# Kernel optimization log

Measured on AMD Instinct MI355X. Metric: run time of the kernel, lower is better.

Reference implementation:

```python
import jax, jax.numpy as jnp
import numpy as np

B, N, FDIM, REL, H = 4, 256, 256, 16, 8
D = FDIM // H


def setup_inputs() -> dict:
    key = jax.random.key(0)
    ks = jax.random.split(key, 10)
    s_f = 1.0 / np.sqrt(FDIM)
    s_kv = 1.0 / np.sqrt(FDIM + REL)
    return {
        "node_features": jax.random.normal(ks[0], (B, N, FDIM), jnp.float32),
        "relative_positions": jax.random.normal(ks[1], (B, N, N, REL), jnp.float32),
        # torch Linear weights stored transposed -> here [in, out]
        "Wq": jax.random.uniform(ks[2], (FDIM, FDIM), jnp.float32, -s_f, s_f),
        "bq": jax.random.uniform(ks[3], (FDIM,), jnp.float32, -s_f, s_f),
        "Wk": jax.random.uniform(ks[4], (FDIM + REL, FDIM), jnp.float32, -s_kv, s_kv),
        "bk": jax.random.uniform(ks[5], (FDIM,), jnp.float32, -s_kv, s_kv),
        "Wv": jax.random.uniform(ks[6], (FDIM + REL, FDIM), jnp.float32, -s_kv, s_kv),
        "bv": jax.random.uniform(ks[7], (FDIM,), jnp.float32, -s_kv, s_kv),
        "Wo": jax.random.uniform(ks[8], (FDIM, FDIM), jnp.float32, -s_f, s_f),
        "bo": jax.random.uniform(ks[9], (FDIM,), jnp.float32, -s_f, s_f),
    }


def reference(node_features, relative_positions, Wq, bq, Wk, bk, Wv, bv, Wo, bo):
    b, n, f = node_features.shape
    # Q: [b, n_i, H, D]
    Q = (node_features @ Wq + bq).reshape(b, n, H, D)
    # per-edge K/V input: [b, i, j, f+rel] where feature part is node j's features
    nf_j = jnp.broadcast_to(node_features[:, None, :, :], (b, n, n, f))
    kv_in = jnp.concatenate([nf_j, relative_positions], axis=-1)
    K = (kv_in @ Wk + bk).reshape(b, n, n, H, D)  # [b, i, j, h, d]
    V = (kv_in @ Wv + bv).reshape(b, n, n, H, D)
    scale = 1.0 / jnp.sqrt(jnp.asarray(D, node_features.dtype))
    scores = jnp.einsum('bihd,bijhd->bhij', Q, K) * scale
    attn = jax.nn.softmax(scores, axis=-1)
    wv = jnp.einsum('bhij,bijhd->bihd', attn, V).reshape(b, n, f)
    return node_features + (wv @ Wo + bo)
```

## Files before the change

### kernel.cpp

```cpp
#include <hip/hip_runtime.h>


#define BB 4
#define NN 256
#define FD 256
#define RL 16
#define NH 8
#define HD 32
#define QI 4

typedef __attribute__((ext_vector_type(8))) short bf16x8;
typedef __attribute__((ext_vector_type(4))) float f32x4;

#define OFF_QB   0
#define OFF_KNA  131072
#define OFF_VNT  262144
#define OFF_NFB  393216
#define OFF_WT   524288

static __device__ __forceinline__ unsigned short f2bf(float x) {
  unsigned int u = __float_as_uint(x);
  unsigned int r = (u + 0x7fffu + ((u >> 16) & 1u)) >> 16;
  return (unsigned short)r;
}
static __device__ __forceinline__ float bf2f(unsigned short h) {
  return __uint_as_float(((unsigned int)h) << 16);
}

__global__ __launch_bounds__(256) void k_prep(
    const float* __restrict__ nf,
    const float* __restrict__ Wq, const float* __restrict__ Wk,
    const float* __restrict__ Wv, const float* __restrict__ Wo,
    float* __restrict__ ws) {
  const int tid = threadIdx.x;
  const int sel = blockIdx.y;
  if (sel == 4) {
    unsigned short* nfB = (unsigned short*)(ws + OFF_NFB);
    const int base = blockIdx.x * 16384;
    #pragma unroll 8
    for (int k = 0; k < 64; ++k) {
      const int idx = base + k * 256 + tid;
      nfB[idx] = f2bf(nf[idx]);
    }
    return;
  }
  const float* W = (sel == 0) ? Wq : (sel == 1) ? Wk : (sel == 2) ? Wv : Wo;
  unsigned short* WT = (unsigned short*)(ws + OFF_WT) + sel * FD * FD;
  __shared__ unsigned short t[64][72];
  const int tx = blockIdx.x & 3, ty = blockIdx.x >> 2;
  const int cx = tid & 63, r0 = tid >> 6;
  #pragma unroll
  for (int rr = r0; rr < 64; rr += 4)
    t[rr][cx] = f2bf(W[(ty * 64 + rr) * FD + tx * 64 + cx]);
  __syncthreads();
  #pragma unroll
  for (int rr = r0; rr < 64; rr += 4)
    WT[(tx * 64 + rr) * FD + ty * 64 + cx] = t[cx][rr];
}

__global__ __launch_bounds__(256) void k_proj(
    const float* __restrict__ bq, const float* __restrict__ bk,
    const float* __restrict__ bv, float* __restrict__ ws) {
  const unsigned short* nfB = (const unsigned short*)(ws + OFF_NFB);
  const int mat = blockIdx.y >> 2;
  const int c0 = (blockIdx.y & 3) * 64;
  const int m0 = blockIdx.x * 64 + (threadIdx.x >> 6) * 16;
  const int l = threadIdx.x & 63;
  const unsigned short* WT = (const unsigned short*)(ws + OFF_WT) + mat * FD * FD;
  const int ar = l & 15, kg = l >> 4;
  f32x4 acc[4];
  #pragma unroll
  for (int nt = 0; nt < 4; ++nt) acc[nt] = (f32x4){0.f, 0.f, 0.f, 0.f};
  #pragma unroll
  for (int ks = 0; ks < 8; ++ks) {
    bf16x8 a = *(const bf16x8*)(nfB + (m0 + ar) * FD + ks * 32 + kg * 8);
    #pragma unroll
    for (int nt = 0; nt < 4; ++nt) {
      bf16x8 b = *(const bf16x8*)(WT + (c0 + nt * 16 + ar) * FD + ks * 32 + kg * 8);
      acc[nt] = __builtin_amdgcn_mfma_f32_16x16x32_bf16(a, b, acc[nt], 0, 0, 0);
    }
  }
  if (mat == 0) {
    const float scale = 0.17677669529663687f;
    unsigned short* Qb = (unsigned short*)(ws + OFF_QB);
    #pragma unroll
    for (int nt = 0; nt < 4; ++nt) {
      const int cc = c0 + nt * 16 + ar;
      const float bb = bq[cc];
      #pragma unroll
      for (int i = 0; i < 4; ++i)
        Qb[(m0 + kg * 4 + i) * FD + cc] = f2bf((acc[nt][i] + bb) * scale);
    }
  } else if (mat == 1) {
    unsigned short* Kn = (unsigned short*)(ws + OFF_KNA);
    #pragma unroll
    for (int nt = 0; nt < 4; ++nt) {
      const int cc = c0 + nt * 16 + ar;
      const float bb = bk[cc];
      #pragma unroll
      for (int i = 0; i < 4; ++i)
        Kn[(m0 + kg * 4 + i) * FD + cc] = f2bf(acc[nt][i] + bb);
    }
  } else {
    unsigned short* VnT = (unsigned short*)(ws + OFF_VNT);
    const int b2 = m0 >> 8, j0 = (m0 & 255) + kg * 4;
    #pragma unroll
    for (int nt = 0; nt < 4; ++nt) {
      const int cc = c0 + nt * 16 + ar;
      const float bb = bv[cc];
      ushort4 v;
      v.x = f2bf(acc[nt][0] + bb); v.y = f2bf(acc[nt][1] + bb);
      v.z = f2bf(acc[nt][2] + bb); v.w = f2bf(acc[nt][3] + bb);
      *(ushort4*)&VnT[((size_t)b2 * FD + cc) * NN + j0] = v;
    }
  }
}

__global__ __launch_bounds__(512, 2) void k_attn11(
    const float* __restrict__ rel,
    const float* __restrict__ Wk,
    const float* __restrict__ Wv,
    const float* __restrict__ nf,
    const float* __restrict__ bo,
    float* __restrict__ out,
    float* __restrict__ ws) {
  const unsigned short* QbG = (const unsigned short*)(ws + OFF_QB);
  const unsigned short* KnG = (const unsigned short*)(ws + OFF_KNA);
  const unsigned short* VTG = (const unsigned short*)(ws + OFF_VNT);
  const unsigned short* WoT = (const unsigned short*)(ws + OFF_WT) + 3 * FD * FD;

  const int bid = (blockIdx.x & 7) * 32 + (blockIdx.x >> 3);
  const int b  = bid >> 6;
  const int i0 = (bid & 63) * QI;
  const int tid = threadIdx.x;
  const int l = tid & 63, w = tid >> 6;
  const int l15 = l & 15, kg = l >> 4;

  __shared__ unsigned short Qb_l[QI * 264];
  __shared__ unsigned short relT[QI * 16 * 264];
  __shared__ unsigned short srelP2[8 * 1064];
  __shared__ float qr_l[QI * 8 * 16];
  __shared__ float ar_l[QI * 8 * 16];
  __shared__ unsigned short wv_l[QI * 264];

  {
    const int t2 = tid * 2, row = t2 >> 8, col = t2 & 255;
    *(unsigned int*)&Qb_l[row * 264 + col] =
        *(const unsigned int*)(QbG + ((size_t)(b * NN + i0 + row)) * FD + col);
  }
  #pragma unroll
  for (int m = 0; m < 2; ++m) {
    const int p = tid + 512 * m, i = p >> 8, j = p & 255;
    const float4* rp = (const float4*)(rel + (((size_t)(b * NN + i0 + i)) * NN + j) * RL);
    #pragma unroll
    for (int q4 = 0; q4 < 4; ++q4) {
      float4 v = rp[q4];
      relT[(i * 16 + q4 * 4 + 0) * 264 + j] = f2bf(v.x);
      relT[(i * 16 + q4 * 4 + 1) * 264 + j] = f2bf(v.y);
      relT[(i * 16 + q4 * 4 + 2) * 264 + j] = f2bf(v.z);
      relT[(i * 16 + q4 * 4 + 3) * 264 + j] = f2bf(v.w);
    }
  }
  __syncthreads();

  {
    const int i = tid >> 7, h = (tid >> 4) & 7, r = tid & 15;
    const unsigned int* qp = (const unsigned int*)&Qb_l[i * 264 + h * 32];
    const float* wrow = Wk + (FD + r) * FD + h * HD;
    float s = 0.f;
    #pragma unroll
    for (int d2 = 0; d2 < 16; ++d2) {
      unsigned int u = qp[d2];
      s += bf2f((unsigned short)(u & 0xffffu)) * wrow[2 * d2];
      s += bf2f((unsigned short)(u >> 16)) * wrow[2 * d2 + 1];
    }
    qr_l[(i * 8 + h) * 16 + r] = s;
  }
  __syncthreads();

  {
    const int i = w & 3, jh = w >> 2;
    const int j0 = jh * 128 + l;
    float rv0[16], rv1[16];
    #pragma unroll
    for (int r = 0; r < 16; ++r) {
      rv0[r] = bf2f(relT[(i * 16 + r) * 264 + j0]);
      rv1[r] = bf2f(relT[(i * 16 + r) * 264 + j0 + 64]);
    }
    #pragma unroll
    for (int h = 0; h < 8; ++h) {
      const float* qv = &qr_l[(i * 8 + h) * 16];
      float s0 = 0.f, s1 = 0.f;
      #pragma unroll
      for (int r = 0; r < 16; ++r) { s0 += qv[r] * rv0[r]; s1 += qv[r] * rv1[r]; }
      srelP2[(i * 8 + h) * 264 + j0]      = f2bf(s0);
      srelP2[(i * 8 + h) * 264 + j0 + 64] = f2bf(s1);
    }
  }
  __syncthreads();

  const int h = w;
  f32x4 acc[16];
  {
    bf16x8 afrag = *(const bf16x8*)&Qb_l[(l15 & 3) * 264 + h * 32 + kg * 8];
    #pragma unroll
    for (int nt = 0; nt < 16; ++nt) {
      bf16x8 bfrag = *(const bf16x8*)(KnG + ((size_t)(b * NN + nt * 16 + l15)) * FD
                                      + h * 32 + kg * 8);
      acc[nt] = __builtin_amdgcn_mfma_f32_16x16x32_bf16(
          afrag, bfrag, (f32x4){0.f, 0.f, 0.f, 0.f}, 0, 0, 0);
    }
    #pragma unroll
    for (int nt = 0; nt < 16; ++nt) {
      #pragma unroll
      for (int ireg = 0; ireg < 4; ++ireg) {
        const int iC = (kg * 4 + ireg) & 3;
        acc[nt][ireg] += bf2f(srelP2[(iC * 8 + h) * 264 + nt * 16 + l15]);
      }
    }
  }
  #pragma unroll
  for (int ireg = 0; ireg < 4; ++ireg) {
    float mx = acc[0][ireg];
    #pragma unroll
    for (int nt = 1; nt < 16; ++nt) mx = fmaxf(mx, acc[nt][ireg]);
    mx = fmaxf(mx, __shfl_xor(mx, 1)); mx = fmaxf(mx, __shfl_xor(mx, 2));
    mx = fmaxf(mx, __shfl_xor(mx, 4)); mx = fmaxf(mx, __shfl_xor(mx, 8));
    float sum = 0.f;
    #pragma unroll
    for (int nt = 0; nt < 16; ++nt) {
      float e = __expf(acc[nt][ireg] - mx);
      acc[nt][ireg] = e; sum += e;
    }
    sum += __shfl_xor(sum, 1); sum += __shfl_xor(sum, 2);
    sum += __shfl_xor(sum, 4); sum += __shfl_xor(sum, 8);
    const float rec = 1.f / sum;
    #pragma unroll
    for (int nt = 0; nt < 16; ++nt) acc[nt][ireg] *= rec;
  }
  __syncthreads();

  if (l < 16) {
    #pragma unroll
    for (int nt = 0; nt < 16; ++nt)
      #pragma unroll
      for (int ireg = 0; ireg < 4; ++ireg)
        srelP2[h * 1064 + ireg * 264 + nt * 16 + l] = f2bf(acc[nt][ireg]);
  }
  __syncthreads();

  if (w < 4) {
    const int i = w;
    const int colh = l15 & 7;
    f32x4 aa = (f32x4){0.f, 0.f, 0.f, 0.f};
    #pragma unroll
    for (int ks = 0; ks < 8; ++ks) {
      bf16x8 a = *(const bf16x8*)&relT[(i * 16 + l15) * 264 + ks * 32 + kg * 8];
      bf16x8 bb = *(const bf16x8*)&srelP2[colh * 1064 + i * 264 + ks * 32 + kg * 8];
      aa = __builtin_amdgcn_mfma_f32_16x16x32_bf16(a, bb, aa, 0, 0, 0);
    }
    if (l15 < 8) {
      #pragma unroll
      for (int ireg = 0; ireg < 4; ++ireg)
        ar_l[(i * 8 + l15) * 16 + kg * 4 + ireg] = aa[ireg];
    }
  }
  __syncthreads();

  {
    const int c = tid & 255, ii0 = tid >> 8, hc = c >> 5;
    float wvv[16];
    #pragma unroll
    for (int r = 0; r < 16; ++r) wvv[r] = Wv[(FD + r) * FD + c];
    #pragma unroll
    for (int k2 = 0; k2 < 2; ++k2) {
      const int i = ii0 + 2 * k2;
      const float* ap = &ar_l[(i * 8 + hc) * 16];
      float s = 0.f;
      #pragma unroll
      for (int r = 0; r < 16; ++r) s += ap[r] * wvv[r];
      wv_l[i * 264 + c] = f2bf(s);
    }
  }
  __syncthreads();

  {
    const int coli = l15 & 3;
    f32x4 o0 = (f32x4){0.f, 0.f, 0.f, 0.f};
    f32x4 o1 = (f32x4){0.f, 0.f, 0.f, 0.f};
    #pragma unroll
    for (int ks = 0; ks < 8; ++ks) {
      bf16x8 bb = *(const bf16x8*)&srelP2[h * 1064 + coli * 264 + ks * 32 + kg * 8];
      bf16x8 a0 = *(const bf16x8*)(VTG + ((size_t)(b * FD + h * 32 + l15)) * NN
                                   + ks * 32 + kg * 8);
      bf16x8 a1 = *(const bf16x8*)(VTG + ((size_t)(b * FD + h * 32 + 16 + l15)) * NN
                                   + ks * 32 + kg * 8);
      o0 = __builtin_amdgcn_mfma_f32_16x16x32_bf16(a0, bb, o0, 0, 0, 0);
      o1 = __builtin_amdgcn_mfma_f32_16x16x32_bf16(a1, bb, o1, 0, 0, 0);
    }
    if (l15 < 4) {
      #pragma unroll
      for (int ireg = 0; ireg < 4; ++ireg) {
        const int c0_ = h * 32 + kg * 4 + ireg;
        const int c1_ = c0_ + 16;
        const int idx0 = l15 * 264 + c0_;
        const int idx1 = l15 * 264 + c1_;
        wv_l[idx0] = f2bf(bf2f(wv_l[idx0]) + o0[ireg]);
        wv_l[idx1] = f2bf(bf2f(wv_l[idx1]) + o1[ireg]);
      }
    }
  }
  __syncthreads();

  {
    const int c0_ = w * 32;
    f32x4 oa0 = (f32x4){0.f, 0.f, 0.f, 0.f};
    f32x4 oa1 = (f32x4){0.f, 0.f, 0.f, 0.f};
    #pragma unroll
    for (int ks = 0; ks < 8; ++ks) {
      bf16x8 a = *(const bf16x8*)&wv_l[(l15 & 3) * 264 + ks * 32 + kg * 8];
      bf16x8 b0 = *(const bf16x8*)(WoT + (c0_ + l15) * FD + ks * 32 + kg * 8);
      bf16x8 b1 = *(const bf16x8*)(WoT + (c0_ + 16 + l15) * FD + ks * 32 + kg * 8);
      oa0 = __builtin_amdgcn_mfma_f32_16x16x32_bf16(a, b0, oa0, 0, 0, 0);
      oa1 = __builtin_amdgcn_mfma_f32_16x16x32_bf16(a, b1, oa1, 0, 0, 0);
    }
    if (l < 16) {
      #pragma unroll
      for (int ireg = 0; ireg < 4; ++ireg) {
        const int row = (b * NN + i0 + ireg) * FD;
        const int cc0 = c0_ + l, cc1 = c0_ + 16 + l;
        out[row + cc0] = nf[row + cc0] + oa0[ireg] + bo[cc0];
        out[row + cc1] = nf[row + cc1] + oa1[ireg] + bo[cc1];
      }
    }
  }
}

extern "C" void kernel_launch(void* const* d_in, const int* in_sizes, int n_in,
                              void* d_out, int out_size, void* d_ws, size_t ws_size,
                              hipStream_t stream) {
  const float* nf  = (const float*)d_in[0];
  const float* rel = (const float*)d_in[1];
  const float* Wq  = (const float*)d_in[2];
  const float* bq  = (const float*)d_in[3];
  const float* Wk  = (const float*)d_in[4];
  const float* bk  = (const float*)d_in[5];
  const float* Wv  = (const float*)d_in[6];
  const float* bv  = (const float*)d_in[7];
  const float* Wo  = (const float*)d_in[8];
  const float* bo  = (const float*)d_in[9];
  float* out = (float*)d_out;
  float* ws  = (float*)d_ws;

  k_prep  <<<dim3(16, 5), 256, 0, stream>>>(nf, Wq, Wk, Wv, Wo, ws);
  k_proj  <<<dim3(16, 12), 256, 0, stream>>>(bq, bk, bv, ws);
  k_attn11<<<BB * NN / QI, 512, 0, stream>>>(rel, Wk, Wv, nf, bo, out, ws);
}
```

Before: 38.27 us.

## Halve query rows per attention block and fuse bf16 conversion into projection

The attention kernel now handles 2 query rows per block instead of 4, which doubles the grid to 512 blocks. All per-block phases (rel transpose, rel-score, score accumulation, AV, output) are re-indexed to match, and the shared scratch shrinks. Separately, the node-feature fp32-to-bf16 conversion moves out of the prep kernel into the projection kernel's operand load, which drops a workspace buffer and one prep pass. The cost is that each MFMA tile now uses only 2 of its 16 rows, and K/V fragments are loaded twice as often overall.

```diff
diff --git a/kernel.cpp b/kernel.cpp
--- a/kernel.cpp
+++ b/kernel.cpp
@@ -7,7 +7,7 @@
 #define RL 16
 #define NH 8
 #define HD 32
-#define QI 4
+#define QI 2
 
 typedef __attribute__((ext_vector_type(8))) short bf16x8;
 typedef __attribute__((ext_vector_type(4))) float f32x4;
@@ -15,8 +15,7 @@
 #define OFF_QB   0
 #define OFF_KNA  131072
 #define OFF_VNT  262144
-#define OFF_NFB  393216
-#define OFF_WT   524288
+#define OFF_WT   393216
 
 static __device__ __forceinline__ unsigned short f2bf(float x) {
   unsigned int u = __float_as_uint(x);
@@ -28,22 +27,11 @@
 }
 
 __global__ __launch_bounds__(256) void k_prep(
-    const float* __restrict__ nf,
     const float* __restrict__ Wq, const float* __restrict__ Wk,
     const float* __restrict__ Wv, const float* __restrict__ Wo,
     float* __restrict__ ws) {
   const int tid = threadIdx.x;
   const int sel = blockIdx.y;
-  if (sel == 4) {
-    unsigned short* nfB = (unsigned short*)(ws + OFF_NFB);
-    const int base = blockIdx.x * 16384;
-    #pragma unroll 8
-    for (int k = 0; k < 64; ++k) {
-      const int idx = base + k * 256 + tid;
-      nfB[idx] = f2bf(nf[idx]);
-    }
-    return;
-  }
   const float* W = (sel == 0) ? Wq : (sel == 1) ? Wk : (sel == 2) ? Wv : Wo;
   unsigned short* WT = (unsigned short*)(ws + OFF_WT) + sel * FD * FD;
   __shared__ unsigned short t[64][72];
@@ -59,9 +47,9 @@
 }
 
 __global__ __launch_bounds__(256) void k_proj(
+    const float* __restrict__ nf,
     const float* __restrict__ bq, const float* __restrict__ bk,
     const float* __restrict__ bv, float* __restrict__ ws) {
-  const unsigned short* nfB = (const unsigned short*)(ws + OFF_NFB);
   const int mat = blockIdx.y >> 2;
   const int c0 = (blockIdx.y & 3) * 64;
   const int m0 = blockIdx.x * 64 + (threadIdx.x >> 6) * 16;
@@ -73,7 +61,14 @@
   for (int nt = 0; nt < 4; ++nt) acc[nt] = (f32x4){0.f, 0.f, 0.f, 0.f};
   #pragma unroll
   for (int ks = 0; ks < 8; ++ks) {
-    bf16x8 a = *(const bf16x8*)(nfB + (m0 + ar) * FD + ks * 32 + kg * 8);
+    const float* nfp = nf + (m0 + ar) * FD + ks * 32 + kg * 8;
+    float4 x0 = *(const float4*)nfp;
+    float4 x1 = *(const float4*)(nfp + 4);
+    bf16x8 a;
+    a[0] = (short)f2bf(x0.x); a[1] = (short)f2bf(x0.y);
+    a[2] = (short)f2bf(x0.z); a[3] = (short)f2bf(x0.w);
+    a[4] = (short)f2bf(x1.x); a[5] = (short)f2bf(x1.y);
+    a[6] = (short)f2bf(x1.z); a[7] = (short)f2bf(x1.w);
     #pragma unroll
     for (int nt = 0; nt < 4; ++nt) {
       bf16x8 b = *(const bf16x8*)(WT + (c0 + nt * 16 + ar) * FD + ks * 32 + kg * 8);
@@ -116,7 +111,7 @@
   }
 }
 
-__global__ __launch_bounds__(512, 2) void k_attn11(
+__global__ __launch_bounds__(512, 2) void k_attn12(
     const float* __restrict__ rel,
     const float* __restrict__ Wk,
     const float* __restrict__ Wv,
@@ -129,28 +124,27 @@
   const unsigned short* VTG = (const unsigned short*)(ws + OFF_VNT);
   const unsigned short* WoT = (const unsigned short*)(ws + OFF_WT) + 3 * FD * FD;
 
-  const int bid = (blockIdx.x & 7) * 32 + (blockIdx.x >> 3);
-  const int b  = bid >> 6;
-  const int i0 = (bid & 63) * QI;
+  const int bid = (blockIdx.x & 7) * 64 + (blockIdx.x >> 3);
+  const int b  = bid >> 7;
+  const int i0 = (bid & 127) * QI;
   const int tid = threadIdx.x;
   const int l = tid & 63, w = tid >> 6;
   const int l15 = l & 15, kg = l >> 4;
 
   __shared__ unsigned short Qb_l[QI * 264];
   __shared__ unsigned short relT[QI * 16 * 264];
-  __shared__ unsigned short srelP2[8 * 1064];
+  __shared__ unsigned short srelP2[16 * 264];
   __shared__ float qr_l[QI * 8 * 16];
   __shared__ float ar_l[QI * 8 * 16];
   __shared__ unsigned short wv_l[QI * 264];
 
-  {
-    const int t2 = tid * 2, row = t2 >> 8, col = t2 & 255;
-    *(unsigned int*)&Qb_l[row * 264 + col] =
-        *(const unsigned int*)(QbG + ((size_t)(b * NN + i0 + row)) * FD + col);
-  }
-  #pragma unroll
-  for (int m = 0; m < 2; ++m) {
-    const int p = tid + 512 * m, i = p >> 8, j = p & 255;
+  if (tid < 256) {
+    const int row = tid >> 7, col2 = tid & 127;
+    *(unsigned int*)&Qb_l[row * 264 + col2 * 2] =
+        *(const unsigned int*)(QbG + ((size_t)(b * NN + i0 + row)) * FD + col2 * 2);
+  }
+  {
+    const int i = tid >> 8, j = tid & 255;
     const float4* rp = (const float4*)(rel + (((size_t)(b * NN + i0 + i)) * NN + j) * RL);
     #pragma unroll
     for (int q4 = 0; q4 < 4; ++q4) {
@@ -163,7 +157,7 @@
   }
   __syncthreads();
 
-  {
+  if (tid < 256) {
     const int i = tid >> 7, h = (tid >> 4) & 7, r = tid & 15;
     const unsigned int* qp = (const unsigned int*)&Qb_l[i * 264 + h * 32];
     const float* wrow = Wk + (FD + r) * FD + h * HD;
@@ -179,22 +173,18 @@
   __syncthreads();
 
   {
-    const int i = w & 3, jh = w >> 2;
-    const int j0 = jh * 128 + l;
-    float rv0[16], rv1[16];
-    #pragma unroll
-    for (int r = 0; r < 16; ++r) {
-      rv0[r] = bf2f(relT[(i * 16 + r) * 264 + j0]);
-      rv1[r] = bf2f(relT[(i * 16 + r) * 264 + j0 + 64]);
-    }
+    const int i = w & 1;
+    const int j0 = (w >> 1) * 64 + l;
+    float rv[16];
+    #pragma unroll
+    for (int r = 0; r < 16; ++r) rv[r] = bf2f(relT[(i * 16 + r) * 264 + j0]);
     #pragma unroll
     for (int h = 0; h < 8; ++h) {
       const float* qv = &qr_l[(i * 8 + h) * 16];
-      float s0 = 0.f, s1 = 0.f;
-      #pragma unroll
-      for (int r = 0; r < 16; ++r) { s0 += qv[r] * rv0[r]; s1 += qv[r] * rv1[r]; }
-      srelP2[(i * 8 + h) * 264 + j0]      = f2bf(s0);
-      srelP2[(i * 8 + h) * 264 + j0 + 64] = f2bf(s1);
+      float s = 0.f;
+      #pragma unroll
+      for (int r = 0; r < 16; ++r) s += qv[r] * rv[r];
+      srelP2[(i * 8 + h) * 264 + j0] = f2bf(s);
     }
   }
   __syncthreads();
@@ -202,7 +192,7 @@
   const int h = w;
   f32x4 acc[16];
   {
-    bf16x8 afrag = *(const bf16x8*)&Qb_l[(l15 & 3) * 264 + h * 32 + kg * 8];
+    bf16x8 afrag = *(const bf16x8*)&Qb_l[(l15 & 1) * 264 + h * 32 + kg * 8];
     #pragma unroll
     for (int nt = 0; nt < 16; ++nt) {
       bf16x8 bfrag = *(const bf16x8*)(KnG + ((size_t)(b * NN + nt * 16 + l15)) * FD
@@ -214,7 +204,7 @@
     for (int nt = 0; nt < 16; ++nt) {
       #pragma unroll
       for (int ireg = 0; ireg < 4; ++ireg) {
-        const int iC = (kg * 4 + ireg) & 3;
+        const int iC = (kg * 4 + ireg) & 1;
         acc[nt][ireg] += bf2f(srelP2[(iC * 8 + h) * 264 + nt * 16 + l15]);
       }
     }
@@ -244,19 +234,19 @@
     #pragma unroll
     for (int nt = 0; nt < 16; ++nt)
       #pragma unroll
-      for (int ireg = 0; ireg < 4; ++ireg)
-        srelP2[h * 1064 + ireg * 264 + nt * 16 + l] = f2bf(acc[nt][ireg]);
-  }
-  __syncthreads();
-
-  if (w < 4) {
+      for (int ireg = 0; ireg < 2; ++ireg)
+        srelP2[h * 528 + ireg * 264 + nt * 16 + l] = f2bf(acc[nt][ireg]);
+  }
+  __syncthreads();
+
+  if (w < 2) {
     const int i = w;
     const int colh = l15 & 7;
     f32x4 aa = (f32x4){0.f, 0.f, 0.f, 0.f};
     #pragma unroll
     for (int ks = 0; ks < 8; ++ks) {
       bf16x8 a = *(const bf16x8*)&relT[(i * 16 + l15) * 264 + ks * 32 + kg * 8];
-      bf16x8 bb = *(const bf16x8*)&srelP2[colh * 1064 + i * 264 + ks * 32 + kg * 8];
+      bf16x8 bb = *(const bf16x8*)&srelP2[colh * 528 + i * 264 + ks * 32 + kg * 8];
       aa = __builtin_amdgcn_mfma_f32_16x16x32_bf16(a, bb, aa, 0, 0, 0);
     }
     if (l15 < 8) {
@@ -268,29 +258,22 @@
   __syncthreads();
 
   {
-    const int c = tid & 255, ii0 = tid >> 8, hc = c >> 5;
-    float wvv[16];
-    #pragma unroll
-    for (int r = 0; r < 16; ++r) wvv[r] = Wv[(FD + r) * FD + c];
-    #pragma unroll
-    for (int k2 = 0; k2 < 2; ++k2) {
-      const int i = ii0 + 2 * k2;
-      const float* ap = &ar_l[(i * 8 + hc) * 16];
-      float s = 0.f;
-      #pragma unroll
-      for (int r = 0; r < 16; ++r) s += ap[r] * wvv[r];
-      wv_l[i * 264 + c] = f2bf(s);
-    }
-  }
-  __syncthreads();
-
-  {
-    const int coli = l15 & 3;
+    const int c = tid & 255, i = tid >> 8, hc = c >> 5;
+    const float* ap = &ar_l[(i * 8 + hc) * 16];
+    float s = 0.f;
+    #pragma unroll
+    for (int r = 0; r < 16; ++r) s += ap[r] * Wv[(FD + r) * FD + c];
+    wv_l[i * 264 + c] = f2bf(s);
+  }
+  __syncthreads();
+
+  {
+    const int coli = l15 & 1;
     f32x4 o0 = (f32x4){0.f, 0.f, 0.f, 0.f};
     f32x4 o1 = (f32x4){0.f, 0.f, 0.f, 0.f};
     #pragma unroll
     for (int ks = 0; ks < 8; ++ks) {
-      bf16x8 bb = *(const bf16x8*)&srelP2[h * 1064 + coli * 264 + ks * 32 + kg * 8];
+      bf16x8 bb = *(const bf16x8*)&srelP2[h * 528 + coli * 264 + ks * 32 + kg * 8];
       bf16x8 a0 = *(const bf16x8*)(VTG + ((size_t)(b * FD + h * 32 + l15)) * NN
                                    + ks * 32 + kg * 8);
       bf16x8 a1 = *(const bf16x8*)(VTG + ((size_t)(b * FD + h * 32 + 16 + l15)) * NN
@@ -298,13 +281,12 @@
       o0 = __builtin_amdgcn_mfma_f32_16x16x32_bf16(a0, bb, o0, 0, 0, 0);
       o1 = __builtin_amdgcn_mfma_f32_16x16x32_bf16(a1, bb, o1, 0, 0, 0);
     }
-    if (l15 < 4) {
+    if (l15 < 2) {
       #pragma unroll
       for (int ireg = 0; ireg < 4; ++ireg) {
         const int c0_ = h * 32 + kg * 4 + ireg;
-        const int c1_ = c0_ + 16;
         const int idx0 = l15 * 264 + c0_;
-        const int idx1 = l15 * 264 + c1_;
+        const int idx1 = l15 * 264 + c0_ + 16;
         wv_l[idx0] = f2bf(bf2f(wv_l[idx0]) + o0[ireg]);
         wv_l[idx1] = f2bf(bf2f(wv_l[idx1]) + o1[ireg]);
       }
@@ -318,7 +300,7 @@
     f32x4 oa1 = (f32x4){0.f, 0.f, 0.f, 0.f};
     #pragma unroll
     for (int ks = 0; ks < 8; ++ks) {
-      bf16x8 a = *(const bf16x8*)&wv_l[(l15 & 3) * 264 + ks * 32 + kg * 8];
+      bf16x8 a = *(const bf16x8*)&wv_l[(l15 & 1) * 264 + ks * 32 + kg * 8];
       bf16x8 b0 = *(const bf16x8*)(WoT + (c0_ + l15) * FD + ks * 32 + kg * 8);
       bf16x8 b1 = *(const bf16x8*)(WoT + (c0_ + 16 + l15) * FD + ks * 32 + kg * 8);
       oa0 = __builtin_amdgcn_mfma_f32_16x16x32_bf16(a, b0, oa0, 0, 0, 0);
@@ -326,7 +308,7 @@
     }
     if (l < 16) {
       #pragma unroll
-      for (int ireg = 0; ireg < 4; ++ireg) {
+      for (int ireg = 0; ireg < 2; ++ireg) {
         const int row = (b * NN + i0 + ireg) * FD;
         const int cc0 = c0_ + l, cc1 = c0_ + 16 + l;
         out[row + cc0] = nf[row + cc0] + oa0[ireg] + bo[cc0];
@@ -352,7 +334,7 @@
   float* out = (float*)d_out;
   float* ws  = (float*)d_ws;
 
-  k_prep  <<<dim3(16, 5), 256, 0, stream>>>(nf, Wq, Wk, Wv, Wo, ws);
-  k_proj  <<<dim3(16, 12), 256, 0, stream>>>(bq, bk, bv, ws);
-  k_attn11<<<BB * NN / QI, 512, 0, stream>>>(rel, Wk, Wv, nf, bo, out, ws);
-}
+  k_prep  <<<dim3(16, 4), 256, 0, stream>>>(Wq, Wk, Wv, Wo, ws);
+  k_proj  <<<dim3(16, 12), 256, 0, stream>>>(nf, bq, bk, bv, ws);
+  k_attn12<<<BB * NN / QI, 512, 0, stream>>>(rel, Wk, Wv, nf, bo, out, ws);
+}
```

Measured after the change: 45.74 us. +19.5%, slower.

## Fuse nf bf16 conversion into projection and prefetch K/V fragments into registers

Applied to the files above, without the earlier changes.

Removes the separate pass that converts node features to bf16 in the prep kernel; the projection kernel now loads fp32 features and converts them inline. The attention kernel issues its global loads of K and V^T fragments early, into registers, so their latency overlaps the rel-position and softmax stages. Launch bounds drop from 2 to 1 blocks per SM to give room for the extra registers. The cost is lower occupancy and redundant conversion of the feature rows across the 12 column blocks of the projection.

```diff
diff --git a/kernel.cpp b/kernel.cpp
--- a/kernel.cpp
+++ b/kernel.cpp
@@ -15,8 +15,7 @@
 #define OFF_QB   0
 #define OFF_KNA  131072
 #define OFF_VNT  262144
-#define OFF_NFB  393216
-#define OFF_WT   524288
+#define OFF_WT   393216
 
 static __device__ __forceinline__ unsigned short f2bf(float x) {
   unsigned int u = __float_as_uint(x);
@@ -28,22 +27,11 @@
 }
 
 __global__ __launch_bounds__(256) void k_prep(
-    const float* __restrict__ nf,
     const float* __restrict__ Wq, const float* __restrict__ Wk,
     const float* __restrict__ Wv, const float* __restrict__ Wo,
     float* __restrict__ ws) {
   const int tid = threadIdx.x;
   const int sel = blockIdx.y;
-  if (sel == 4) {
-    unsigned short* nfB = (unsigned short*)(ws + OFF_NFB);
-    const int base = blockIdx.x * 16384;
-    #pragma unroll 8
-    for (int k = 0; k < 64; ++k) {
-      const int idx = base + k * 256 + tid;
-      nfB[idx] = f2bf(nf[idx]);
-    }
-    return;
-  }
   const float* W = (sel == 0) ? Wq : (sel == 1) ? Wk : (sel == 2) ? Wv : Wo;
   unsigned short* WT = (unsigned short*)(ws + OFF_WT) + sel * FD * FD;
   __shared__ unsigned short t[64][72];
@@ -59,9 +47,9 @@
 }
 
 __global__ __launch_bounds__(256) void k_proj(
+    const float* __restrict__ nf,
     const float* __restrict__ bq, const float* __restrict__ bk,
     const float* __restrict__ bv, float* __restrict__ ws) {
-  const unsigned short* nfB = (const unsigned short*)(ws + OFF_NFB);
   const int mat = blockIdx.y >> 2;
   const int c0 = (blockIdx.y & 3) * 64;
   const int m0 = blockIdx.x * 64 + (threadIdx.x >> 6) * 16;
@@ -73,7 +61,14 @@
   for (int nt = 0; nt < 4; ++nt) acc[nt] = (f32x4){0.f, 0.f, 0.f, 0.f};
   #pragma unroll
   for (int ks = 0; ks < 8; ++ks) {
-    bf16x8 a = *(const bf16x8*)(nfB + (m0 + ar) * FD + ks * 32 + kg * 8);
+    const float* nfp = nf + (m0 + ar) * FD + ks * 32 + kg * 8;
+    float4 x0 = *(const float4*)nfp;
+    float4 x1 = *(const float4*)(nfp + 4);
+    bf16x8 a;
+    a[0] = (short)f2bf(x0.x); a[1] = (short)f2bf(x0.y);
+    a[2] = (short)f2bf(x0.z); a[3] = (short)f2bf(x0.w);
+    a[4] = (short)f2bf(x1.x); a[5] = (short)f2bf(x1.y);
+    a[6] = (short)f2bf(x1.z); a[7] = (short)f2bf(x1.w);
     #pragma unroll
     for (int nt = 0; nt < 4; ++nt) {
       bf16x8 b = *(const bf16x8*)(WT + (c0 + nt * 16 + ar) * FD + ks * 32 + kg * 8);
@@ -116,7 +111,7 @@
   }
 }
 
-__global__ __launch_bounds__(512, 2) void k_attn11(
+__global__ __launch_bounds__(512, 1) void k_attn13(
     const float* __restrict__ rel,
     const float* __restrict__ Wk,
     const float* __restrict__ Wv,
@@ -135,6 +130,7 @@
   const int tid = threadIdx.x;
   const int l = tid & 63, w = tid >> 6;
   const int l15 = l & 15, kg = l >> 4;
+  const int h = w;
 
   __shared__ unsigned short Qb_l[QI * 264];
   __shared__ unsigned short relT[QI * 16 * 264];
@@ -143,6 +139,12 @@
   __shared__ float ar_l[QI * 8 * 16];
   __shared__ unsigned short wv_l[QI * 264];
 
+  bf16x8 knpf[16];
+  #pragma unroll
+  for (int nt = 0; nt < 16; ++nt)
+    knpf[nt] = *(const bf16x8*)(KnG + ((size_t)(b * NN + nt * 16 + l15)) * FD
+                                + h * 32 + kg * 8);
+
   {
     const int t2 = tid * 2, row = t2 >> 8, col = t2 & 255;
     *(unsigned int*)&Qb_l[row * 264 + col] =
@@ -164,9 +166,9 @@
   __syncthreads();
 
   {
-    const int i = tid >> 7, h = (tid >> 4) & 7, r = tid & 15;
-    const unsigned int* qp = (const unsigned int*)&Qb_l[i * 264 + h * 32];
-    const float* wrow = Wk + (FD + r) * FD + h * HD;
+    const int i = tid >> 7, hq = (tid >> 4) & 7, r = tid & 15;
+    const unsigned int* qp = (const unsigned int*)&Qb_l[i * 264 + hq * 32];
+    const float* wrow = Wk + (FD + r) * FD + hq * HD;
     float s = 0.f;
     #pragma unroll
     for (int d2 = 0; d2 < 16; ++d2) {
@@ -174,7 +176,7 @@
       s += bf2f((unsigned short)(u & 0xffffu)) * wrow[2 * d2];
       s += bf2f((unsigned short)(u >> 16)) * wrow[2 * d2 + 1];
     }
-    qr_l[(i * 8 + h) * 16 + r] = s;
+    qr_l[(i * 8 + hq) * 16 + r] = s;
   }
   __syncthreads();
 
@@ -188,27 +190,24 @@
       rv1[r] = bf2f(relT[(i * 16 + r) * 264 + j0 + 64]);
     }
     #pragma unroll
-    for (int h = 0; h < 8; ++h) {
-      const float* qv = &qr_l[(i * 8 + h) * 16];
+    for (int hh = 0; hh < 8; ++hh) {
+      const float* qv = &qr_l[(i * 8 + hh) * 16];
       float s0 = 0.f, s1 = 0.f;
       #pragma unroll
       for (int r = 0; r < 16; ++r) { s0 += qv[r] * rv0[r]; s1 += qv[r] * rv1[r]; }
-      srelP2[(i * 8 + h) * 264 + j0]      = f2bf(s0);
-      srelP2[(i * 8 + h) * 264 + j0 + 64] = f2bf(s1);
-    }
-  }
-  __syncthreads();
-
-  const int h = w;
+      srelP2[(i * 8 + hh) * 264 + j0]      = f2bf(s0);
+      srelP2[(i * 8 + hh) * 264 + j0 + 64] = f2bf(s1);
+    }
+  }
+  __syncthreads();
+
   f32x4 acc[16];
   {
     bf16x8 afrag = *(const bf16x8*)&Qb_l[(l15 & 3) * 264 + h * 32 + kg * 8];
     #pragma unroll
     for (int nt = 0; nt < 16; ++nt) {
-      bf16x8 bfrag = *(const bf16x8*)(KnG + ((size_t)(b * NN + nt * 16 + l15)) * FD
-                                      + h * 32 + kg * 8);
       acc[nt] = __builtin_amdgcn_mfma_f32_16x16x32_bf16(
-          afrag, bfrag, (f32x4){0.f, 0.f, 0.f, 0.f}, 0, 0, 0);
+          afrag, knpf[nt], (f32x4){0.f, 0.f, 0.f, 0.f}, 0, 0, 0);
     }
     #pragma unroll
     for (int nt = 0; nt < 16; ++nt) {
@@ -247,6 +246,15 @@
       for (int ireg = 0; ireg < 4; ++ireg)
         srelP2[h * 1064 + ireg * 264 + nt * 16 + l] = f2bf(acc[nt][ireg]);
   }
+
+  bf16x8 vpf0[8], vpf1[8];
+  #pragma unroll
+  for (int ks = 0; ks < 8; ++ks) {
+    vpf0[ks] = *(const bf16x8*)(VTG + ((size_t)(b * FD + h * 32 + l15)) * NN
+                                + ks * 32 + kg * 8);
+    vpf1[ks] = *(const bf16x8*)(VTG + ((size_t)(b * FD + h * 32 + 16 + l15)) * NN
+                                + ks * 32 + kg * 8);
+  }
   __syncthreads();
 
   if (w < 4) {
@@ -291,20 +299,15 @@
     #pragma unroll
     for (int ks = 0; ks < 8; ++ks) {
       bf16x8 bb = *(const bf16x8*)&srelP2[h * 1064 + coli * 264 + ks * 32 + kg * 8];
-      bf16x8 a0 = *(const bf16x8*)(VTG + ((size_t)(b * FD + h * 32 + l15)) * NN
-                                   + ks * 32 + kg * 8);
-      bf16x8 a1 = *(const bf16x8*)(VTG + ((size_t)(b * FD + h * 32 + 16 + l15)) * NN
-                                   + ks * 32 + kg * 8);
-      o0 = __builtin_amdgcn_mfma_f32_16x16x32_bf16(a0, bb, o0, 0, 0, 0);
-      o1 = __builtin_amdgcn_mfma_f32_16x16x32_bf16(a1, bb, o1, 0, 0, 0);
+      o0 = __builtin_amdgcn_mfma_f32_16x16x32_bf16(vpf0[ks], bb, o0, 0, 0, 0);
+      o1 = __builtin_amdgcn_mfma_f32_16x16x32_bf16(vpf1[ks], bb, o1, 0, 0, 0);
     }
     if (l15 < 4) {
       #pragma unroll
       for (int ireg = 0; ireg < 4; ++ireg) {
         const int c0_ = h * 32 + kg * 4 + ireg;
-        const int c1_ = c0_ + 16;
         const int idx0 = l15 * 264 + c0_;
-        const int idx1 = l15 * 264 + c1_;
+        const int idx1 = l15 * 264 + c0_ + 16;
         wv_l[idx0] = f2bf(bf2f(wv_l[idx0]) + o0[ireg]);
         wv_l[idx1] = f2bf(bf2f(wv_l[idx1]) + o1[ireg]);
       }
@@ -352,7 +355,7 @@
   float* out = (float*)d_out;
   float* ws  = (float*)d_ws;
 
-  k_prep  <<<dim3(16, 5), 256, 0, stream>>>(nf, Wq, Wk, Wv, Wo, ws);
-  k_proj  <<<dim3(16, 12), 256, 0, stream>>>(bq, bk, bv, ws);
-  k_attn11<<<BB * NN / QI, 512, 0, stream>>>(rel, Wk, Wv, nf, bo, out, ws);
-}
+  k_prep  <<<dim3(16, 4), 256, 0, stream>>>(Wq, Wk, Wv, Wo, ws);
+  k_proj  <<<dim3(16, 12), 256, 0, stream>>>(nf, bq, bk, bv, ws);
+  k_attn13<<<BB * NN / QI, 512, 0, stream>>>(rel, Wk, Wv, nf, bo, out, ws);
+}
```

After: 38.02 us. No clear change (-0.7%).
